# Kernel tuning notes

Hardware: AMD Instinct MI355X
Metric: run time of the kernel (lower is better)

Reference implementation:

```python
import jax, jax.numpy as jnp
import numpy as np

N_NODES = 20000
N_EDGES = 160000
N_GRAPHS = 64
DIMS = [9, 128, 256, 512, 1534]
NEG_SLOPE_ATT = 0.2   # GATConv attention LeakyReLU
NEG_SLOPE_ACT = 0.01  # nn.LeakyReLU between layers
EPS = 1e-5            # GraphNorm eps


def setup_inputs() -> dict:
    key = jax.random.key(0)
    inp = {}
    k, key = jax.random.split(key)
    inp['x'] = jax.random.normal(k, (N_NODES, DIMS[0]), jnp.float32)
    k, key = jax.random.split(key)
    inp['edge_index'] = jax.random.randint(k, (2, N_EDGES), 0, N_NODES)
    k, key = jax.random.split(key)
    inp['batch'] = jnp.sort(jax.random.randint(k, (N_NODES,), 0, N_GRAPHS))
    for l in range(4):
        din, dout = DIMS[l], DIMS[l + 1]
        k1, k2, k3, key = jax.random.split(key, 4)
        s = 1.0 / np.sqrt(din)
        inp[f'W{l}'] = (jax.random.normal(k1, (din, dout)) * s).astype(jnp.float32)
        inp[f'asrc{l}'] = (jax.random.normal(k2, (dout,)) * 0.1).astype(jnp.float32)
        inp[f'adst{l}'] = (jax.random.normal(k3, (dout,)) * 0.1).astype(jnp.float32)
        inp[f'b{l}'] = jnp.zeros((dout,), jnp.float32)
        inp[f'g{l}'] = jnp.ones((dout,), jnp.float32)   # GraphNorm weight
        inp[f'bt{l}'] = jnp.zeros((dout,), jnp.float32)  # GraphNorm bias
        inp[f'ms{l}'] = jnp.ones((dout,), jnp.float32)   # GraphNorm mean_scale
    return inp


def _gat_conv(h, src, dst, n, W, asrc, adst, b):
    # PyG GATConv, heads=1: linear (no bias), edge attention, segment softmax, scatter-add
    hp = h @ W                                                    # [N, dout]
    e = jax.nn.leaky_relu((hp @ asrc)[src] + (hp @ adst)[dst], NEG_SLOPE_ATT)  # [E]
    m = jax.ops.segment_max(e, dst, num_segments=n)
    m = jnp.where(jnp.isfinite(m), m, 0.0)
    ex = jnp.exp(e - m[dst])
    denom = jax.ops.segment_sum(ex, dst, num_segments=n)
    alpha = ex / (denom[dst] + 1e-16)                             # [E]
    out = jax.ops.segment_sum(alpha[:, None] * hp[src], dst, num_segments=n)
    return out + b


def _graph_norm(h, batch, counts, g, bt, ms):
    # PyG GraphNorm: per-graph mean/var with learnable mean_scale
    mean = jax.ops.segment_sum(h, batch, num_segments=N_GRAPHS) / counts
    out = h - ms * mean[batch]
    var = jax.ops.segment_sum(out * out, batch, num_segments=N_GRAPHS) / counts
    return out / jnp.sqrt(var[batch] + EPS) * g + bt


def _forward(x, edge_index, batch, params):
    n = x.shape[0]
    loops = jnp.arange(n)
    src = jnp.concatenate([edge_index[0], loops])   # GATConv add_self_loops=True
    dst = jnp.concatenate([edge_index[1], loops])
    counts = jax.ops.segment_sum(jnp.ones((n,), x.dtype), batch, num_segments=N_GRAPHS)[:, None]
    h = x
    for (W, asrc, adst, b, g, bt, ms) in params:
        h = _gat_conv(h, src, dst, n, W, asrc, adst, b)
        h = jax.nn.leaky_relu(h, NEG_SLOPE_ACT)
        h = _graph_norm(h, batch, counts, g, bt, ms)
        # Dropout(p=0.1) is identity in eval mode
    mean = (jax.ops.segment_sum(h, batch, num_segments=N_GRAPHS) / counts)[:, None, :]
    mx = jax.ops.segment_max(h, batch, num_segments=N_GRAPHS)[:, None, :]
    return jnp.concatenate([mean, mx], axis=1)      # [G, 2, 1534]


def reference(x, edge_index, batch,
              W0, asrc0, adst0, b0, g0, bt0, ms0,
              W1, asrc1, adst1, b1, g1, bt1, ms1,
              W2, asrc2, adst2, b2, g2, bt2, ms2,
              W3, asrc3, adst3, b3, g3, bt3, ms3):
    params = [
        (W0, asrc0, adst0, b0, g0, bt0, ms0),
        (W1, asrc1, adst1, b1, g1, bt1, ms1),
        (W2, asrc2, adst2, b2, g2, bt2, ms2),
        (W3, asrc3, adst3, b3, g3, bt3, ms3),
    ]
    return _forward(x, edge_index, batch, params)
```

## Files before the change

kernel.cpp:

```cpp
#include <hip/hip_runtime.h>
#include <math.h>

typedef unsigned int u32;
typedef unsigned short u16;
using half8 = __attribute__((ext_vector_type(8))) _Float16;
using f32x4 = __attribute__((ext_vector_type(4))) float;

#define NN 20000
#define MPAD 20096
#define NE 160000
#define ET 180000
#define NG 64
#define NBLK 79

constexpr float NEG_ATT = 0.2f;
constexpr float NEG_ACT = 0.01f;
constexpr float EPS_GN  = 1e-5f;

struct Ptr4 { const float *p0, *p1, *p2, *p3; };


__device__ __forceinline__ u16 f2h(float f) {
    _Float16 h = (_Float16)f;
    return __builtin_bit_cast(u16, h);
}
__device__ __forceinline__ float h2f(u16 b) {
    return (float)__builtin_bit_cast(_Float16, b);
}

__device__ __forceinline__ void gl_lds16(const void* g, void* l) {
    __builtin_amdgcn_global_load_lds((const __attribute__((address_space(1))) u32*)g,
                                     (__attribute__((address_space(3))) u32*)l, 16, 0, 0);
}

__device__ __forceinline__ float lrelu_att(float v) {
    return (v > 0.f) ? v : NEG_ATT * v;
}


__global__ void k_bounds(const int* __restrict__ batch, int* __restrict__ counts,
                         int* __restrict__ gstart) {
    __shared__ int ls[NG + 1];
    int g = threadIdx.x;
    int lo = 0, hi = NN;
    while (lo < hi) {
        int mid = (lo + hi) >> 1;
        if (batch[mid] < g) lo = mid + 1; else hi = mid;
    }
    ls[g] = lo;
    if (g == 0) ls[NG] = NN;
    __syncthreads();
    counts[g] = ls[g + 1] - ls[g];
    gstart[g] = ls[g];
    if (g == 0) gstart[NG] = NN;
}


__global__ void k_deg(const int* __restrict__ ei, int* deg) {
    int i = blockIdx.x * 256 + threadIdx.x;
    if (i >= ET) return;
    int dst = (i < NE) ? ei[NE + i] : (i - NE);
    atomicAdd(&deg[dst], 1);
}

__global__ void k_scan1(const int* __restrict__ deg, int* __restrict__ bsum) {
    int i = blockIdx.x * 256 + threadIdx.x;
    int v = (i < NN) ? deg[i] : 0;
    int lane = threadIdx.x & 63, w = threadIdx.x >> 6;
    #pragma unroll
    for (int off = 32; off; off >>= 1) v += __shfl_down(v, off, 64);
    __shared__ int ws[4];
    if (lane == 0) ws[w] = v;
    __syncthreads();
    if (threadIdx.x == 0) bsum[blockIdx.x] = ws[0] + ws[1] + ws[2] + ws[3];
}

__global__ void k_scan2(const int* __restrict__ bsum, int* __restrict__ boff,
                        int* __restrict__ total) {
    int tid = threadIdx.x;
    int v = (tid < NBLK) ? bsum[tid] : 0;
    int lane = tid & 63, w = tid >> 6;
    int val = v;
    #pragma unroll
    for (int off = 1; off < 64; off <<= 1) {
        int t = __shfl_up(val, off, 64);
        if (lane >= off) val += t;
    }
    __shared__ int ws[4];
    if (lane == 63) ws[w] = val;
    __syncthreads();
    int woff = 0;
    for (int k = 0; k < w; k++) woff += ws[k];
    int excl = woff + val - v;
    if (tid < NBLK) boff[tid] = excl;
    if (tid == NBLK - 1) *total = excl + v;
}

__global__ void k_scan3(const int* __restrict__ deg, const int* __restrict__ boff,
                        int* __restrict__ row_ptr, int* __restrict__ cursor) {
    int i = blockIdx.x * 256 + threadIdx.x;
    int v = (i < NN) ? deg[i] : 0;
    int lane = threadIdx.x & 63, w = threadIdx.x >> 6;
    int val = v;
    #pragma unroll
    for (int off = 1; off < 64; off <<= 1) {
        int t = __shfl_up(val, off, 64);
        if (lane >= off) val += t;
    }
    __shared__ int ws[4];
    if (lane == 63) ws[w] = val;
    __syncthreads();
    int woff = 0;
    for (int k = 0; k < w; k++) woff += ws[k];
    int excl = boff[blockIdx.x] + woff + val - v;
    if (i < NN) { row_ptr[i] = excl; cursor[i] = excl; }
}

__global__ void k_scatter(const int* __restrict__ ei, int* cursor, int* __restrict__ col) {
    int i = blockIdx.x * 256 + threadIdx.x;
    if (i >= ET) return;
    int s, d;
    if (i < NE) { s = ei[i]; d = ei[NE + i]; } else { s = i - NE; d = s; }
    int p = atomicAdd(&cursor[d], 1);
    col[p] = s;
}


__global__ void k_wvec_all(Ptr4 W, Ptr4 As, Ptr4 Ad,
                           float* __restrict__ wsrcA, float* __restrict__ wdstA) {
    const int dins[4]  = {9, 128, 256, 512};
    const int douts[4] = {128, 256, 512, 1534};
    int l = blockIdx.y, k = blockIdx.x;
    if (k >= dins[l]) return;
    const float* Wp = (l == 0) ? W.p0 : (l == 1) ? W.p1 : (l == 2) ? W.p2 : W.p3;
    const float* as = (l == 0) ? As.p0 : (l == 1) ? As.p1 : (l == 2) ? As.p2 : As.p3;
    const float* ad = (l == 0) ? Ad.p0 : (l == 1) ? Ad.p1 : (l == 2) ? Ad.p2 : Ad.p3;
    int NC = douts[l];
    const float* row = Wp + (size_t)k * NC;
    float ss = 0.f, sd = 0.f;
    for (int n = threadIdx.x; n < NC; n += 256) {
        float w = row[n];
        ss += w * as[n];
        sd += w * ad[n];
    }
    __shared__ float ls[8];
    int lane = threadIdx.x & 63, w4 = threadIdx.x >> 6;
    #pragma unroll
    for (int off = 32; off; off >>= 1) {
        ss += __shfl_down(ss, off, 64);
        sd += __shfl_down(sd, off, 64);
    }
    if (lane == 0) { ls[w4] = ss; ls[4 + w4] = sd; }
    __syncthreads();
    if (threadIdx.x == 0) {
        wsrcA[l * 512 + k] = ls[0] + ls[1] + ls[2] + ls[3];
        wdstA[l * 512 + k] = ls[4] + ls[5] + ls[6] + ls[7];
    }
}


__global__ void k_wbt_all(Ptr4 W, u16* __restrict__ WbTall) {
    const int Ks[3] = {128, 256, 512};
    const int NCs[3] = {256, 512, 1534};
    const int Nps[3] = {256, 512, 1536};
    const size_t offs[3] = {0, 256 * 128, 256 * 128 + 512 * 256};
    int l = blockIdx.z;
    int K = Ks[l], NC = NCs[l], Np = Nps[l];
    int n0 = blockIdx.x * 32, k0 = blockIdx.y * 32;
    if (n0 >= Np || k0 >= K) return;
    const float* Wp = (l == 0) ? W.p1 : (l == 1) ? W.p2 : W.p3;
    u16* WbT = WbTall + offs[l];
    __shared__ u16 tile[32][33];
    int tx = threadIdx.x & 31, ty = threadIdx.x >> 5;
    #pragma unroll
    for (int i = 0; i < 4; i++) {
        int k = k0 + ty + i * 8, n = n0 + tx;
        float v = (k < K && n < NC) ? Wp[(size_t)k * NC + n] : 0.f;
        tile[ty + i * 8][tx] = f2h(v);
    }
    __syncthreads();
    #pragma unroll
    for (int i = 0; i < 4; i++) {
        int n = n0 + ty + i * 8, k = k0 + tx;
        if (n < Np && k < K) WbT[(size_t)n * K + k] = tile[tx][ty + i * 8];
    }
}


__global__ void k_scores0(const float* __restrict__ x, const float* __restrict__ wsrc,
                          const float* __restrict__ wdst, float* __restrict__ s_src,
                          float* __restrict__ s_dst) {
    int v = blockIdx.x * 256 + threadIdx.x;
    if (v >= NN) return;
    const float* r = x + (size_t)v * 9;
    float ss = 0.f, sd = 0.f;
    #pragma unroll
    for (int k = 0; k < 9; k++) { ss += r[k] * wsrc[k]; sd += r[k] * wdst[k]; }
    s_src[v] = ss; s_dst[v] = sd;
}

template <int VW>
__global__ void k_scores_h(const u16* __restrict__ h, const float* __restrict__ wsrc,
                           const float* __restrict__ wdst, float* __restrict__ s_src,
                           float* __restrict__ s_dst, int din) {
    int v = blockIdx.x * 4 + (threadIdx.x >> 6);
    int lane = threadIdx.x & 63;
    if (v >= NN) return;
    const u16* row = h + (size_t)v * din;
    float ss = 0.f, sd = 0.f;
    for (int d = lane * VW; d < din; d += 64 * VW) {
        u32 ua[VW / 2];
        if constexpr (VW == 2) {
            ua[0] = *(const u32*)(row + d);
        } else if constexpr (VW == 4) {
            uint2 t = *(const uint2*)(row + d);
            ua[0] = t.x; ua[1] = t.y;
        } else {
            uint4 t = *(const uint4*)(row + d);
            ua[0] = t.x; ua[1] = t.y; ua[2] = t.z; ua[3] = t.w;
        }
        #pragma unroll
        for (int j = 0; j < VW / 2; j++) {
            float h0 = h2f((u16)(ua[j] & 0xffffu)), h1 = h2f((u16)(ua[j] >> 16));
            ss += h0 * wsrc[d + 2 * j] + h1 * wsrc[d + 2 * j + 1];
            sd += h0 * wdst[d + 2 * j] + h1 * wdst[d + 2 * j + 1];
        }
    }
    #pragma unroll
    for (int off = 32; off; off >>= 1) {
        ss += __shfl_down(ss, off, 64);
        sd += __shfl_down(sd, off, 64);
    }
    if (lane == 0) { s_src[v] = ss; s_dst[v] = sd; }
}


template <int TPN, int CPT>
__global__ __launch_bounds__(256) void k_agg_fused(const u16* __restrict__ h,
                                                   const int* __restrict__ row_ptr,
                                                   const int* __restrict__ col,
                                                   const float* __restrict__ s_src,
                                                   const float* __restrict__ s_dst,
                                                   u16* __restrict__ agg, int din) {
    constexpr int NPB = 256 / TPN;
    __shared__ float sm[NPB * 2];
    int grp = threadIdx.x / TPN;
    int lane = threadIdx.x % TPN;
    int v = blockIdx.x * NPB + grp;
    bool valid = v < NN;
    int st = 0, en = 0;
    float sd = 0.f;
    if (valid) { st = row_ptr[v]; en = row_ptr[v + 1]; sd = s_dst[v]; }

    float mx = -INFINITY;
    if (valid && lane < 64) {
        for (int p = st + lane; p < en; p += 64)
            mx = fmaxf(mx, lrelu_att(s_src[col[p]] + sd));
    }
    #pragma unroll
    for (int off = 32; off; off >>= 1) mx = fmaxf(mx, __shfl_xor(mx, off, 64));
    float sum = 0.f;
    if (valid && lane < 64) {
        for (int p = st + lane; p < en; p += 64)
            sum += __expf(lrelu_att(s_src[col[p]] + sd) - mx);
    }
    #pragma unroll
    for (int off = 32; off; off >>= 1) sum += __shfl_xor(sum, off, 64);
    if (lane == 0) { sm[grp * 2] = mx; sm[grp * 2 + 1] = 1.0f / (sum + 1e-16f); }
    __syncthreads();
    if (!valid) return;
    float m = sm[grp * 2], inv = sm[grp * 2 + 1];

    int d0 = lane * 2 * CPT;
    float acc[2 * CPT];
    #pragma unroll
    for (int i = 0; i < 2 * CPT; i++) acc[i] = 0.f;
    const u16* hb = h + d0;
    int p = st;
    for (; p + 2 <= en; p += 2) {
        int c0 = col[p], c1 = col[p + 1];
        float a0 = __expf(lrelu_att(s_src[c0] + sd) - m);
        float a1 = __expf(lrelu_att(s_src[c1] + sd) - m);
        u32 u0[CPT], u1[CPT];
        if constexpr (CPT == 1) {
            u0[0] = *(const u32*)(hb + (size_t)c0 * din);
            u1[0] = *(const u32*)(hb + (size_t)c1 * din);
        } else {
            uint2 t0 = *(const uint2*)(hb + (size_t)c0 * din);
            uint2 t1 = *(const uint2*)(hb + (size_t)c1 * din);
            u0[0] = t0.x; u0[1] = t0.y; u1[0] = t1.x; u1[1] = t1.y;
        }
        #pragma unroll
        for (int wv = 0; wv < CPT; wv++) {
            acc[2 * wv]     += a0 * h2f((u16)(u0[wv] & 0xffffu)) + a1 * h2f((u16)(u1[wv] & 0xffffu));
            acc[2 * wv + 1] += a0 * h2f((u16)(u0[wv] >> 16))     + a1 * h2f((u16)(u1[wv] >> 16));
        }
    }
    if (p < en) {
        int c0 = col[p];
        float a0 = __expf(lrelu_att(s_src[c0] + sd) - m);
        u32 u0[CPT];
        if constexpr (CPT == 1) {
            u0[0] = *(const u32*)(hb + (size_t)c0 * din);
        } else {
            uint2 t0 = *(const uint2*)(hb + (size_t)c0 * din);
            u0[0] = t0.x; u0[1] = t0.y;
        }
        #pragma unroll
        for (int wv = 0; wv < CPT; wv++) {
            acc[2 * wv]     += a0 * h2f((u16)(u0[wv] & 0xffffu));
            acc[2 * wv + 1] += a0 * h2f((u16)(u0[wv] >> 16));
        }
    }
    u32 o[CPT];
    #pragma unroll
    for (int wv = 0; wv < CPT; wv++)
        o[wv] = (u32)f2h(acc[2 * wv] * inv) | ((u32)f2h(acc[2 * wv + 1] * inv) << 16);
    if constexpr (CPT == 1) {
        *(u32*)(agg + (size_t)v * din + d0) = o[0];
    } else {
        uint2 ov; ov.x = o[0]; ov.y = o[1];
        *(uint2*)(agg + (size_t)v * din + d0) = ov;
    }
}

__global__ __launch_bounds__(256) void k_agg0_fused(const float* __restrict__ x,
                                                    const int* __restrict__ row_ptr,
                                                    const int* __restrict__ col,
                                                    const float* __restrict__ s_src,
                                                    const float* __restrict__ s_dst,
                                                    float* __restrict__ agg0) {
    __shared__ float sm[4 * 2];
    int grp = threadIdx.x >> 6;
    int lane = threadIdx.x & 63;
    int v = blockIdx.x * 4 + grp;
    bool valid = v < NN;
    int st = 0, en = 0;
    float sd = 0.f;
    if (valid) { st = row_ptr[v]; en = row_ptr[v + 1]; sd = s_dst[v]; }
    float mx = -INFINITY;
    if (valid) {
        for (int p = st + lane; p < en; p += 64)
            mx = fmaxf(mx, lrelu_att(s_src[col[p]] + sd));
    }
    #pragma unroll
    for (int off = 32; off; off >>= 1) mx = fmaxf(mx, __shfl_xor(mx, off, 64));
    float sum = 0.f;
    if (valid) {
        for (int p = st + lane; p < en; p += 64)
            sum += __expf(lrelu_att(s_src[col[p]] + sd) - mx);
    }
    #pragma unroll
    for (int off = 32; off; off >>= 1) sum += __shfl_xor(sum, off, 64);
    if (lane == 0) { sm[grp * 2] = mx; sm[grp * 2 + 1] = 1.0f / (sum + 1e-16f); }
    __syncthreads();
    if (!valid || lane >= 9) return;
    float m = sm[grp * 2], inv = sm[grp * 2 + 1];
    float acc = 0.f;
    for (int p = st; p < en; p++) {
        int c = col[p];
        float a = __expf(lrelu_att(s_src[c] + sd) - m);
        acc += a * x[(size_t)c * 9 + lane];
    }
    agg0[(size_t)v * 9 + lane] = acc * inv;
}


__global__ __launch_bounds__(256) void k_gemm0(const float* __restrict__ agg0,
                                               const float* __restrict__ W,
                                               const float* __restrict__ bias,
                                               u16* __restrict__ out) {
    __shared__ float Ws[9 * 128];
    for (int i = threadIdx.x; i < 9 * 128; i += 256) Ws[i] = W[i];
    __syncthreads();
    int node = blockIdx.x * 2 + (threadIdx.x >> 7);
    int n = threadIdx.x & 127;
    if (node >= NN) return;
    const float* xr = agg0 + (size_t)node * 9;
    float acc = bias[n];
    #pragma unroll
    for (int k = 0; k < 9; k++) acc += xr[k] * Ws[k * 128 + n];
    acc = (acc > 0.f) ? acc : NEG_ACT * acc;
    out[(size_t)node * 128 + n] = f2h(acc);
}


#define BM 128
#define BK 32

__global__ __launch_bounds__(256) void k_gemm_f16(const u16* __restrict__ A,
                                                  const u16* __restrict__ B,
                                                  const float* __restrict__ bias,
                                                  u16* __restrict__ C,
                                                  int K, int ldC, int NC, int ntx) {
    int nwg = gridDim.x;
    int b = blockIdx.x;
    int q = nwg >> 3, r = nwg & 7;
    int xcd = b & 7, idx = b >> 3;
    int wg = (xcd < r ? xcd * (q + 1) : r * (q + 1) + (xcd - r) * q) + idx;
    int row0 = (wg / ntx) * BM;
    int col0 = (wg % ntx) * BM;

    __shared__ u16 lds[2][2][BM * BK];
    int tid = threadIdx.x;
    int lane = tid & 63, w = tid >> 6;
    int wr = w >> 1, wc = w & 1;

    f32x4 acc[4][4];
    #pragma unroll
    for (int m = 0; m < 4; m++)
        #pragma unroll
        for (int n = 0; n < 4; n++)
            #pragma unroll
            for (int rr2 = 0; rr2 < 4; rr2++) acc[m][n][rr2] = 0.f;

    int nt = K / BK;

    auto stage = [&](int buf, int t) {
        int k0 = t * BK;
        #pragma unroll
        for (int c = 0; c < 2; c++) {
            int idx2 = tid + c * 256;
            int rr2 = idx2 >> 2, kc = idx2 & 3;
            int kcs = kc ^ (rr2 & 3);
            gl_lds16(A + (size_t)(row0 + rr2) * K + k0 + kcs * 8, &lds[buf][0][idx2 * 8]);
            gl_lds16(B + (size_t)(col0 + rr2) * K + k0 + kcs * 8, &lds[buf][1][idx2 * 8]);
        }
    };

    auto compute = [&](int buf) {
        const u16* As = &lds[buf][0][0];
        const u16* Bs = &lds[buf][1][0];
        int kg = lane >> 4, rl = lane & 15;
        half8 af[4], bfr[4];
        #pragma unroll
        for (int m = 0; m < 4; m++) {
            int rr2 = wr * 64 + m * 16 + rl;
            af[m] = *(const half8*)(As + rr2 * BK + (kg ^ (rr2 & 3)) * 8);
        }
        #pragma unroll
        for (int n = 0; n < 4; n++) {
            int rr2 = wc * 64 + n * 16 + rl;
            bfr[n] = *(const half8*)(Bs + rr2 * BK + (kg ^ (rr2 & 3)) * 8);
        }
        #pragma unroll
        for (int m = 0; m < 4; m++)
            #pragma unroll
            for (int n = 0; n < 4; n++)
                acc[m][n] = __builtin_amdgcn_mfma_f32_16x16x32_f16(af[m], bfr[n], acc[m][n], 0, 0, 0);
    };

    stage(0, 0);
    __syncthreads();
    for (int t = 0; t < nt; t++) {
        if (t + 1 < nt) stage((t + 1) & 1, t + 1);
        compute(t & 1);
        __syncthreads();
    }

    u16* ep = ((u16*)lds) + w * (32 * 72);
    int kg = lane >> 4, rl = lane & 15;
    int rrow = lane >> 3;
    int c8 = (lane & 7) * 8;
    #pragma unroll
    for (int half = 0; half < 2; half++) {
        #pragma unroll
        for (int m2 = 0; m2 < 2; m2++) {
            int m = half * 2 + m2;
            #pragma unroll
            for (int n = 0; n < 4; n++) {
                int colg = col0 + wc * 64 + n * 16 + rl;
                float bb = (colg < NC) ? bias[colg] : 0.f;
                #pragma unroll
                for (int rr2 = 0; rr2 < 4; rr2++) {
                    float o = acc[m][n][rr2] + bb;
                    o = (o > 0.f) ? o : NEG_ACT * o;
                    ep[(m2 * 16 + kg * 4 + rr2) * 72 + n * 16 + rl] = f2h(o);
                }
            }
        }
        #pragma unroll
        for (int it = 0; it < 4; it++) {
            int rloc = it * 8 + rrow;
            half8 vv = *(const half8*)(ep + rloc * 72 + c8);
            int rowg = row0 + wr * 64 + half * 32 + rloc;
            *(half8*)(C + (size_t)rowg * ldC + col0 + wc * 64 + c8) = vv;
        }
    }
}


__global__ __launch_bounds__(1024, 4) void k_gemm256(const u16* __restrict__ A,
                                                     const u16* __restrict__ B,
                                                     const float* __restrict__ bias,
                                                     u16* __restrict__ C,
                                                     int K, int ldC, int NC, int ntx, int M) {
    __shared__ u16 sMem[49152];

    int nwg = gridDim.x, b = blockIdx.x;
    int q = nwg >> 3, r = nwg & 7;
    int xcd = b & 7, bidx = b >> 3;
    int wg = (xcd < r ? xcd * (q + 1) : r * (q + 1) + (xcd - r) * q) + bidx;
    int row0 = (wg / ntx) * 256;
    int col0 = (wg % ntx) * 256;

    int tid = threadIdx.x;
    int w = tid >> 6, lane = tid & 63;
    int wm = w >> 2, wn = w & 3;
    int rl = lane & 15, kg = lane >> 4;
    int ksl = (kg ^ ((rl >> 1) & 3)) * 8;

    f32x4 acc[4][4];
    #pragma unroll
    for (int m = 0; m < 4; m++)
        #pragma unroll
        for (int n = 0; n < 4; n++)
            #pragma unroll
            for (int i = 0; i < 4; i++) acc[m][n][i] = 0.f;

    {
        int rr = tid >> 2, s = tid & 3;
        int ss = s ^ ((rr >> 1) & 3);
        int ra = row0 + rr; ra = (ra < M) ? ra : (M - 1);
        const u16* aSrc0 = A + (size_t)ra * K + ss * 8;
        const u16* bSrc0 = B + (size_t)(col0 + rr) * K + ss * 8;
        u16* dstA = sMem + tid * 8;
        u16* dstB = sMem + 8192 + tid * 8;

        auto stage = [&](int t, int bf2) {
            gl_lds16(aSrc0 + t * 32, dstA + bf2 * 16384);
            gl_lds16(bSrc0 + t * 32, dstB + bf2 * 16384);
        };

        half8 af[4], bf[4];
        auto ldAB = [&](int bf2) {
            const u16* Ab = sMem + bf2 * 16384;
            const u16* Bb = Ab + 8192;
            #pragma unroll
            for (int i = 0; i < 4; i++)
                af[i] = *(const half8*)(Ab + (wm * 64 + i * 16 + rl) * 32 + ksl);
            #pragma unroll
            for (int i = 0; i < 4; i++)
                bf[i] = *(const half8*)(Bb + (wn * 64 + i * 16 + rl) * 32 + ksl);
        };

        int nt = K >> 5;

        stage(0, 0); stage(1, 1);
        __builtin_amdgcn_sched_barrier(0);
        asm volatile("s_waitcnt vmcnt(2)" ::: "memory");
        __builtin_amdgcn_s_barrier();
        __builtin_amdgcn_sched_barrier(0);

        int rb = 0;
        for (int t = 0; t < nt; t++) {
            int sb = rb + 2; if (sb >= 3) sb -= 3;
            if (t + 2 < nt) stage(t + 2, sb);
            ldAB(rb);
            __builtin_amdgcn_s_setprio(1);
            #pragma unroll
            for (int i = 0; i < 4; i++)
                #pragma unroll
                for (int n = 0; n < 4; n++)
                    acc[i][n] = __builtin_amdgcn_mfma_f32_16x16x32_f16(af[i], bf[n], acc[i][n], 0, 0, 0);
            __builtin_amdgcn_s_setprio(0);
            __builtin_amdgcn_sched_barrier(0);
            if (t + 2 < nt)      asm volatile("s_waitcnt vmcnt(2)" ::: "memory");
            else if (t + 1 < nt) asm volatile("s_waitcnt vmcnt(0)" ::: "memory");
            __builtin_amdgcn_s_barrier();
            __builtin_amdgcn_sched_barrier(0);
            rb = (rb == 2) ? 0 : rb + 1;
        }
    }

    u16* ep = sMem + w * (32 * 72);
    float bv[4];
    #pragma unroll
    for (int n = 0; n < 4; n++) {
        int colg = col0 + wn * 64 + n * 16 + rl;
        bv[n] = (colg < NC) ? bias[colg] : 0.f;
    }
    int rrow = lane >> 3, c8 = (lane & 7) * 8;
    #pragma unroll
    for (int mh = 0; mh < 2; mh++) {
        #pragma unroll
        for (int msub = 0; msub < 2; msub++) {
            int m = mh * 2 + msub;
            #pragma unroll
            for (int n = 0; n < 4; n++) {
                #pragma unroll
                for (int rg = 0; rg < 4; rg++) {
                    float o = acc[m][n][rg] + bv[n];
                    o = (o > 0.f) ? o : NEG_ACT * o;
                    ep[(msub * 16 + kg * 4 + rg) * 72 + n * 16 + rl] = f2h(o);
                }
            }
        }
        #pragma unroll
        for (int it = 0; it < 4; it++) {
            int rloc = it * 8 + rrow;
            half8 vv = *(const half8*)(ep + rloc * 72 + c8);
            int rowg = row0 + wm * 64 + mh * 32 + rloc;
            if (rowg < M)
                *(half8*)(C + (size_t)rowg * ldC + col0 + wn * 64 + c8) = vv;
        }
    }
}


__global__ __launch_bounds__(256) void k_gn_fused(const u16* __restrict__ h,
                           const int* __restrict__ gstart,
                           const float* __restrict__ ms, const float* __restrict__ gam,
                           const float* __restrict__ bet, u16* __restrict__ out, int ld) {
    int g = blockIdx.x;
    int c0 = blockIdx.y * 128;
    int ct = threadIdx.x & 15, rg = threadIdx.x >> 4;
    int d0 = c0 + ct * 8;
    int st = gstart[g], en = gstart[g + 1];
    float inv = 1.0f / (float)(en - st);
    float s[8], qq[8];
    #pragma unroll
    for (int i = 0; i < 8; i++) { s[i] = 0.f; qq[i] = 0.f; }
    for (int r = st + rg; r < en; r += 16) {
        uint4 u = *(const uint4*)(h + (size_t)r * ld + d0);
        u32 ua[4] = {u.x, u.y, u.z, u.w};
        #pragma unroll
        for (int j = 0; j < 4; j++) {
            float v0 = h2f((u16)(ua[j] & 0xffffu)), v1 = h2f((u16)(ua[j] >> 16));
            s[2 * j] += v0; s[2 * j + 1] += v1;
            qq[2 * j] += v0 * v0; qq[2 * j + 1] += v1 * v1;
        }
    }
    __shared__ float Ls[16][128], Lq[16][128];
    #pragma unroll
    for (int i = 0; i < 8; i++) { Ls[rg][ct * 8 + i] = s[i]; Lq[rg][ct * 8 + i] = qq[i]; }
    __syncthreads();
    int tid = threadIdx.x;
    if (tid < 128) {
        float ss = 0.f, sq = 0.f;
        #pragma unroll
        for (int r2 = 1; r2 < 16; r2++) { ss += Ls[r2][tid]; sq += Lq[r2][tid]; }
        Ls[0][tid] += ss; Lq[0][tid] += sq;
    }
    __syncthreads();
    float sub[8], sc[8], bv[8];
    #pragma unroll
    for (int i = 0; i < 8; i++) {
        int cl = ct * 8 + i, d = d0 + i;
        float msv = ms[d];
        float mean = Ls[0][cl] * inv;
        float q2   = Lq[0][cl] * inv;
        float var  = fmaxf(q2 - (2.f * msv - msv * msv) * mean * mean, 0.f);
        sub[i] = msv * mean;
        sc[i]  = gam[d] * rsqrtf(var + EPS_GN);
        bv[i]  = bet[d];
    }
    for (int r = st + rg; r < en; r += 16) {
        uint4 u = *(const uint4*)(h + (size_t)r * ld + d0);
        u32 ua[4] = {u.x, u.y, u.z, u.w};
        uint4 wv4;
        u32 wo[4];
        #pragma unroll
        for (int j = 0; j < 4; j++) {
            float o0 = (h2f((u16)(ua[j] & 0xffffu)) - sub[2 * j]) * sc[2 * j] + bv[2 * j];
            float o1 = (h2f((u16)(ua[j] >> 16)) - sub[2 * j + 1]) * sc[2 * j + 1] + bv[2 * j + 1];
            wo[j] = (u32)f2h(o0) | ((u32)f2h(o1) << 16);
        }
        wv4.x = wo[0]; wv4.y = wo[1]; wv4.z = wo[2]; wv4.w = wo[3];
        *(uint4*)(out + (size_t)r * ld + d0) = wv4;
    }
}

__global__ __launch_bounds__(256) void k_gn_poolf(const u16* __restrict__ h,
                           const int* __restrict__ gstart,
                           const float* __restrict__ ms, const float* __restrict__ gam,
                           const float* __restrict__ bet, float* __restrict__ out,
                           int dout, int ld) {
    int g = blockIdx.x;
    int c0 = blockIdx.y * 128;
    int ct = threadIdx.x & 15, rg = threadIdx.x >> 4;
    int d0 = c0 + ct * 8;
    int st = gstart[g], en = gstart[g + 1];
    float inv = 1.0f / (float)(en - st);
    float s[8], qq[8];
    #pragma unroll
    for (int i = 0; i < 8; i++) { s[i] = 0.f; qq[i] = 0.f; }
    for (int r = st + rg; r < en; r += 16) {
        uint4 u = *(const uint4*)(h + (size_t)r * ld + d0);
        u32 ua[4] = {u.x, u.y, u.z, u.w};
        #pragma unroll
        for (int j = 0; j < 4; j++) {
            float v0 = h2f((u16)(ua[j] & 0xffffu)), v1 = h2f((u16)(ua[j] >> 16));
            s[2 * j] += v0; s[2 * j + 1] += v1;
            qq[2 * j] += v0 * v0; qq[2 * j + 1] += v1 * v1;
        }
    }
    __shared__ float Ls[16][128], Lq[16][128];
    #pragma unroll
    for (int i = 0; i < 8; i++) { Ls[rg][ct * 8 + i] = s[i]; Lq[rg][ct * 8 + i] = qq[i]; }
    __syncthreads();
    int tid = threadIdx.x;
    if (tid < 128) {
        float ss = 0.f, sq = 0.f;
        #pragma unroll
        for (int r2 = 1; r2 < 16; r2++) { ss += Ls[r2][tid]; sq += Lq[r2][tid]; }
        Ls[0][tid] += ss; Lq[0][tid] += sq;
    }
    __syncthreads();
    float sub[8], sc[8], bv[8];
    #pragma unroll
    for (int i = 0; i < 8; i++) {
        int cl = ct * 8 + i, d = d0 + i;
        int dc = (d < dout) ? d : (dout - 1);
        float msv = ms[dc];
        float mean = Ls[0][cl] * inv;
        float q2   = Lq[0][cl] * inv;
        float var  = fmaxf(q2 - (2.f * msv - msv * msv) * mean * mean, 0.f);
        sub[i] = msv * mean;
        sc[i]  = gam[dc] * rsqrtf(var + EPS_GN);
        bv[i]  = bet[dc];
    }
    float ps[8], pm[8];
    #pragma unroll
    for (int i = 0; i < 8; i++) { ps[i] = 0.f; pm[i] = -INFINITY; }
    for (int r = st + rg; r < en; r += 16) {
        uint4 u = *(const uint4*)(h + (size_t)r * ld + d0);
        u32 ua[4] = {u.x, u.y, u.z, u.w};
        #pragma unroll
        for (int j = 0; j < 4; j++) {
            float o0 = (h2f((u16)(ua[j] & 0xffffu)) - sub[2 * j]) * sc[2 * j] + bv[2 * j];
            float o1 = (h2f((u16)(ua[j] >> 16)) - sub[2 * j + 1]) * sc[2 * j + 1] + bv[2 * j + 1];
            ps[2 * j] += o0; ps[2 * j + 1] += o1;
            pm[2 * j] = fmaxf(pm[2 * j], o0); pm[2 * j + 1] = fmaxf(pm[2 * j + 1], o1);
        }
    }
    __syncthreads();
    #pragma unroll
    for (int i = 0; i < 8; i++) { Ls[rg][ct * 8 + i] = ps[i]; Lq[rg][ct * 8 + i] = pm[i]; }
    __syncthreads();
    if (tid < 128) {
        float ss = 0.f, mm = -INFINITY;
        #pragma unroll
        for (int r2 = 0; r2 < 16; r2++) { ss += Ls[r2][tid]; mm = fmaxf(mm, Lq[r2][tid]); }
        int d = c0 + tid;
        if (d < dout) {
            out[(size_t)g * 2 * dout + d] = ss * inv;
            out[(size_t)g * 2 * dout + dout + d] = mm;
        }
    }
}


extern "C" void kernel_launch(void* const* d_in, const int* in_sizes, int n_in,
                              void* d_out, int out_size, void* d_ws, size_t ws_size,
                              hipStream_t stream) {
    const float* x = (const float*)d_in[0];
    const int* ei = (const int*)d_in[1];
    const int* batch = (const int*)d_in[2];
    const float *Wl[4], *Asr[4], *Ads[4], *Bi[4], *Ga[4], *Be[4], *Ms[4];
    for (int l = 0; l < 4; l++) {
        int b = 3 + 7 * l;
        Wl[l]  = (const float*)d_in[b];
        Asr[l] = (const float*)d_in[b + 1];
        Ads[l] = (const float*)d_in[b + 2];
        Bi[l]  = (const float*)d_in[b + 3];
        Ga[l]  = (const float*)d_in[b + 4];
        Be[l]  = (const float*)d_in[b + 5];
        Ms[l]  = (const float*)d_in[b + 6];
    }

    char* ws = (char*)d_ws;
    size_t off = 0;
    auto alloc = [&](size_t bytes) -> char* {
        char* p = ws + off;
        off += (bytes + 255) & ~(size_t)255;
        return p;
    };
    u16*   actA   = (u16*)alloc((size_t)MPAD * 512 * 2);
    u16*   actB   = (u16*)alloc((size_t)MPAD * 1536 * 2);
    u16*   agg    = (u16*)alloc((size_t)MPAD * 512 * 2);
    float* agg0   = (float*)alloc((size_t)NN * 9 * 4);
    u16*   WbTall = (u16*)alloc((size_t)(256 * 128 + 512 * 256 + 1536 * 512) * 2);
    float* wsrcA  = (float*)alloc((size_t)4 * 512 * 4);
    float* wdstA  = (float*)alloc((size_t)4 * 512 * 4);
    float* s_src  = (float*)alloc((size_t)NN * 4);
    float* s_dst  = (float*)alloc((size_t)NN * 4);
    int* row_ptr  = (int*)alloc((size_t)(NN + 1) * 4);
    int* cursor   = (int*)alloc((size_t)NN * 4);
    int* colA     = (int*)alloc((size_t)ET * 4);
    int* counts   = (int*)alloc((size_t)NG * 4);
    int* gstart   = (int*)alloc((size_t)(NG + 1) * 4);
    int* bsum     = (int*)alloc((size_t)NBLK * 4);
    int* boff     = (int*)alloc((size_t)NBLK * 4);

    char* zbase = ws + off;
    int* deg      = (int*)alloc((size_t)NN * 4);
    size_t zbytes = (size_t)((ws + off) - zbase);
    hipMemsetAsync(zbase, 0, zbytes, stream);

    k_bounds<<<1, 64, 0, stream>>>(batch, counts, gstart);
    k_deg<<<(ET + 255) / 256, 256, 0, stream>>>(ei, deg);
    k_scan1<<<NBLK, 256, 0, stream>>>(deg, bsum);
    k_scan2<<<1, 256, 0, stream>>>(bsum, boff, row_ptr + NN);
    k_scan3<<<NBLK, 256, 0, stream>>>(deg, boff, row_ptr, cursor);
    k_scatter<<<(ET + 255) / 256, 256, 0, stream>>>(ei, cursor, colA);

    Ptr4 Wp{Wl[0], Wl[1], Wl[2], Wl[3]};
    Ptr4 Ap{Asr[0], Asr[1], Asr[2], Asr[3]};
    Ptr4 Dp{Ads[0], Ads[1], Ads[2], Ads[3]};
    k_wvec_all<<<dim3(512, 4), 256, 0, stream>>>(Wp, Ap, Dp, wsrcA, wdstA);
    k_wbt_all<<<dim3(48, 16, 3), 256, 0, stream>>>(Wp, WbTall);

    const int dims[5] = {9, 128, 256, 512, 1534};
    const size_t wbtOffs[3] = {0, 256 * 128, 256 * 128 + 512 * 256};
    const int RT256 = (MPAD + 255) / 256;

    for (int l = 0; l < 4; l++) {
        int din = dims[l], dout = dims[l + 1];
        int ldo = (dout == 1534) ? 1536 : dout;
        const float* wsrc = wsrcA + l * 512;
        const float* wdst = wdstA + l * 512;

        if (l == 0) {
            k_scores0<<<(NN + 255) / 256, 256, 0, stream>>>(x, wsrc, wdst, s_src, s_dst);
            k_agg0_fused<<<(NN + 3) / 4, 256, 0, stream>>>(x, row_ptr, colA, s_src, s_dst, agg0);
            k_gemm0<<<(NN + 1) / 2, 256, 0, stream>>>(agg0, Wl[0], Bi[0], actB);
        } else if (l == 1) {
            k_scores_h<2><<<(NN + 3) / 4, 256, 0, stream>>>(actA, wsrc, wdst, s_src, s_dst, din);
            k_agg_fused<64, 1><<<(NN + 3) / 4, 256, 0, stream>>>(actA, row_ptr, colA, s_src, s_dst, agg, din);
            int ntx = ldo / 128;
            int nwg = ntx * (MPAD / 128);
            k_gemm_f16<<<nwg, 256, 0, stream>>>(agg, WbTall + wbtOffs[0], Bi[1], actB,
                                                din, ldo, dout, ntx);
        } else {
            if (din == 256) {
                k_scores_h<4><<<(NN + 3) / 4, 256, 0, stream>>>(actA, wsrc, wdst, s_src, s_dst, din);
                k_agg_fused<64, 2><<<(NN + 3) / 4, 256, 0, stream>>>(actA, row_ptr, colA, s_src, s_dst, agg, din);
            } else {
                k_scores_h<8><<<(NN + 3) / 4, 256, 0, stream>>>(actA, wsrc, wdst, s_src, s_dst, din);
                k_agg_fused<128, 2><<<(NN + 1) / 2, 256, 0, stream>>>(actA, row_ptr, colA, s_src, s_dst, agg, din);
            }
            int ntx = ldo / 256;
            int nwg = ntx * RT256;
            k_gemm256<<<nwg, 1024, 0, stream>>>(agg, WbTall + wbtOffs[l - 1], Bi[l], actB,
                                                din, ldo, dout, ntx, MPAD);
        }

        if (l < 3)
            k_gn_fused<<<dim3(NG, ldo / 128), 256, 0, stream>>>(actB, gstart,
                                                                Ms[l], Ga[l], Be[l], actA, ldo);
        else
            k_gn_poolf<<<dim3(NG, 12), 256, 0, stream>>>(actB, gstart,
                                                         Ms[3], Ga[3], Be[3], (float*)d_out,
                                                         1534, 1536);
    }
}
```

Before: 332.9 us.

## Split GAT aggregation into alpha precompute and column-chunked gather kernels

The fused softmax+aggregation kernel is replaced by two kernels. The first computes per-edge normalized attention weights into a global buffer, and the second gathers neighbor features in 64-column chunks with 16 threads per node and 16 nodes per block. This removes the repeated exp/score recomputation per feature lane and the block-level sync, and gives many more small blocks with better occupancy. In exchange it adds an extra launch, an alpha buffer write and read, and repeated col/alpha reads for each column chunk.

```diff
diff --git a/kernel.cpp b/kernel.cpp
--- a/kernel.cpp
+++ b/kernel.cpp
@@ -235,93 +235,74 @@
 }
 
 
-template <int TPN, int CPT>
-__global__ __launch_bounds__(256) void k_agg_fused(const u16* __restrict__ h,
-                                                   const int* __restrict__ row_ptr,
-                                                   const int* __restrict__ col,
-                                                   const float* __restrict__ s_src,
-                                                   const float* __restrict__ s_dst,
-                                                   u16* __restrict__ agg, int din) {
-    constexpr int NPB = 256 / TPN;
-    __shared__ float sm[NPB * 2];
-    int grp = threadIdx.x / TPN;
-    int lane = threadIdx.x % TPN;
-    int v = blockIdx.x * NPB + grp;
-    bool valid = v < NN;
-    int st = 0, en = 0;
-    float sd = 0.f;
-    if (valid) { st = row_ptr[v]; en = row_ptr[v + 1]; sd = s_dst[v]; }
-
+__global__ __launch_bounds__(256) void k_alpha(const int* __restrict__ row_ptr,
+                                               const int* __restrict__ col,
+                                               const float* __restrict__ s_src,
+                                               const float* __restrict__ s_dst,
+                                               float* __restrict__ alpha) {
+    int grp = threadIdx.x >> 6;
+    int lane = threadIdx.x & 63;
+    int v = blockIdx.x * 4 + grp;
+    if (v >= NN) return;
+    int st = row_ptr[v], en = row_ptr[v + 1];
+    float sd = s_dst[v];
     float mx = -INFINITY;
-    if (valid && lane < 64) {
-        for (int p = st + lane; p < en; p += 64)
-            mx = fmaxf(mx, lrelu_att(s_src[col[p]] + sd));
-    }
+    for (int p = st + lane; p < en; p += 64)
+        mx = fmaxf(mx, lrelu_att(s_src[col[p]] + sd));
     #pragma unroll
     for (int off = 32; off; off >>= 1) mx = fmaxf(mx, __shfl_xor(mx, off, 64));
     float sum = 0.f;
-    if (valid && lane < 64) {
-        for (int p = st + lane; p < en; p += 64)
-            sum += __expf(lrelu_att(s_src[col[p]] + sd) - mx);
-    }
+    for (int p = st + lane; p < en; p += 64)
+        sum += __expf(lrelu_att(s_src[col[p]] + sd) - mx);
     #pragma unroll
     for (int off = 32; off; off >>= 1) sum += __shfl_xor(sum, off, 64);
-    if (lane == 0) { sm[grp * 2] = mx; sm[grp * 2 + 1] = 1.0f / (sum + 1e-16f); }
-    __syncthreads();
-    if (!valid) return;
-    float m = sm[grp * 2], inv = sm[grp * 2 + 1];
-
-    int d0 = lane * 2 * CPT;
-    float acc[2 * CPT];
-    #pragma unroll
-    for (int i = 0; i < 2 * CPT; i++) acc[i] = 0.f;
+    float inv = 1.0f / (sum + 1e-16f);
+    for (int p = st + lane; p < en; p += 64)
+        alpha[p] = __expf(lrelu_att(s_src[col[p]] + sd) - mx) * inv;
+}
+
+
+__global__ __launch_bounds__(256) void k_agg_gather(const u16* __restrict__ h,
+                                                    const int* __restrict__ row_ptr,
+                                                    const int* __restrict__ col,
+                                                    const float* __restrict__ alpha,
+                                                    u16* __restrict__ agg,
+                                                    int din, int nbn) {
+    int blk = blockIdx.x;
+    int chunk = blk / nbn;
+    int nb = blk % nbn;
+    int tg = threadIdx.x >> 4;
+    int lane = threadIdx.x & 15;
+    int v = nb * 16 + tg;
+    if (v >= NN) return;
+    int st = row_ptr[v], en = row_ptr[v + 1];
+    int d0 = chunk * 64 + lane * 4;
     const u16* hb = h + d0;
+    float a0_, a1_, acc0 = 0.f, acc1 = 0.f, acc2 = 0.f, acc3 = 0.f;
     int p = st;
     for (; p + 2 <= en; p += 2) {
         int c0 = col[p], c1 = col[p + 1];
-        float a0 = __expf(lrelu_att(s_src[c0] + sd) - m);
-        float a1 = __expf(lrelu_att(s_src[c1] + sd) - m);
-        u32 u0[CPT], u1[CPT];
-        if constexpr (CPT == 1) {
-            u0[0] = *(const u32*)(hb + (size_t)c0 * din);
-            u1[0] = *(const u32*)(hb + (size_t)c1 * din);
-        } else {
-            uint2 t0 = *(const uint2*)(hb + (size_t)c0 * din);
-            uint2 t1 = *(const uint2*)(hb + (size_t)c1 * din);
-            u0[0] = t0.x; u0[1] = t0.y; u1[0] = t1.x; u1[1] = t1.y;
-        }
-        #pragma unroll
-        for (int wv = 0; wv < CPT; wv++) {
-            acc[2 * wv]     += a0 * h2f((u16)(u0[wv] & 0xffffu)) + a1 * h2f((u16)(u1[wv] & 0xffffu));
-            acc[2 * wv + 1] += a0 * h2f((u16)(u0[wv] >> 16))     + a1 * h2f((u16)(u1[wv] >> 16));
-        }
+        a0_ = alpha[p]; a1_ = alpha[p + 1];
+        uint2 t0 = *(const uint2*)(hb + (size_t)c0 * din);
+        uint2 t1 = *(const uint2*)(hb + (size_t)c1 * din);
+        acc0 += a0_ * h2f((u16)(t0.x & 0xffffu)) + a1_ * h2f((u16)(t1.x & 0xffffu));
+        acc1 += a0_ * h2f((u16)(t0.x >> 16))     + a1_ * h2f((u16)(t1.x >> 16));
+        acc2 += a0_ * h2f((u16)(t0.y & 0xffffu)) + a1_ * h2f((u16)(t1.y & 0xffffu));
+        acc3 += a0_ * h2f((u16)(t0.y >> 16))     + a1_ * h2f((u16)(t1.y >> 16));
     }
     if (p < en) {
         int c0 = col[p];
-        float a0 = __expf(lrelu_att(s_src[c0] + sd) - m);
-        u32 u0[CPT];
-        if constexpr (CPT == 1) {
-            u0[0] = *(const u32*)(hb + (size_t)c0 * din);
-        } else {
-            uint2 t0 = *(const uint2*)(hb + (size_t)c0 * din);
-            u0[0] = t0.x; u0[1] = t0.y;
-        }
-        #pragma unroll
-        for (int wv = 0; wv < CPT; wv++) {
-            acc[2 * wv]     += a0 * h2f((u16)(u0[wv] & 0xffffu));
-            acc[2 * wv + 1] += a0 * h2f((u16)(u0[wv] >> 16));
-        }
-    }
-    u32 o[CPT];
-    #pragma unroll
-    for (int wv = 0; wv < CPT; wv++)
-        o[wv] = (u32)f2h(acc[2 * wv] * inv) | ((u32)f2h(acc[2 * wv + 1] * inv) << 16);
-    if constexpr (CPT == 1) {
-        *(u32*)(agg + (size_t)v * din + d0) = o[0];
-    } else {
-        uint2 ov; ov.x = o[0]; ov.y = o[1];
-        *(uint2*)(agg + (size_t)v * din + d0) = ov;
-    }
+        a0_ = alpha[p];
+        uint2 t0 = *(const uint2*)(hb + (size_t)c0 * din);
+        acc0 += a0_ * h2f((u16)(t0.x & 0xffffu));
+        acc1 += a0_ * h2f((u16)(t0.x >> 16));
+        acc2 += a0_ * h2f((u16)(t0.y & 0xffffu));
+        acc3 += a0_ * h2f((u16)(t0.y >> 16));
+    }
+    uint2 ov;
+    ov.x = (u32)f2h(acc0) | ((u32)f2h(acc1) << 16);
+    ov.y = (u32)f2h(acc2) | ((u32)f2h(acc3) << 16);
+    *(uint2*)(agg + (size_t)v * din + d0) = ov;
 }
 
 __global__ __launch_bounds__(256) void k_agg0_fused(const float* __restrict__ x,
@@ -785,6 +766,7 @@
     float* wdstA  = (float*)alloc((size_t)4 * 512 * 4);
     float* s_src  = (float*)alloc((size_t)NN * 4);
     float* s_dst  = (float*)alloc((size_t)NN * 4);
+    float* alpha  = (float*)alloc((size_t)ET * 4);
     int* row_ptr  = (int*)alloc((size_t)(NN + 1) * 4);
     int* cursor   = (int*)alloc((size_t)NN * 4);
     int* colA     = (int*)alloc((size_t)ET * 4);
@@ -814,6 +796,7 @@
     const int dims[5] = {9, 128, 256, 512, 1534};
     const size_t wbtOffs[3] = {0, 256 * 128, 256 * 128 + 512 * 256};
     const int RT256 = (MPAD + 255) / 256;
+    const int NBN = (NN + 15) / 16;
 
     for (int l = 0; l < 4; l++) {
         int din = dims[l], dout = dims[l + 1];
@@ -825,25 +808,28 @@
             k_scores0<<<(NN + 255) / 256, 256, 0, stream>>>(x, wsrc, wdst, s_src, s_dst);
             k_agg0_fused<<<(NN + 3) / 4, 256, 0, stream>>>(x, row_ptr, colA, s_src, s_dst, agg0);
             k_gemm0<<<(NN + 1) / 2, 256, 0, stream>>>(agg0, Wl[0], Bi[0], actB);
-        } else if (l == 1) {
-            k_scores_h<2><<<(NN + 3) / 4, 256, 0, stream>>>(actA, wsrc, wdst, s_src, s_dst, din);
-            k_agg_fused<64, 1><<<(NN + 3) / 4, 256, 0, stream>>>(actA, row_ptr, colA, s_src, s_dst, agg, din);
-            int ntx = ldo / 128;
-            int nwg = ntx * (MPAD / 128);
-            k_gemm_f16<<<nwg, 256, 0, stream>>>(agg, WbTall + wbtOffs[0], Bi[1], actB,
-                                                din, ldo, dout, ntx);
         } else {
-            if (din == 256) {
+            if (din == 128)
+                k_scores_h<2><<<(NN + 3) / 4, 256, 0, stream>>>(actA, wsrc, wdst, s_src, s_dst, din);
+            else if (din == 256)
                 k_scores_h<4><<<(NN + 3) / 4, 256, 0, stream>>>(actA, wsrc, wdst, s_src, s_dst, din);
-                k_agg_fused<64, 2><<<(NN + 3) / 4, 256, 0, stream>>>(actA, row_ptr, colA, s_src, s_dst, agg, din);
+            else
+                k_scores_h<8><<<(NN + 3) / 4, 256, 0, stream>>>(actA, wsrc, wdst, s_src, s_dst, din);
+            k_alpha<<<(NN + 3) / 4, 256, 0, stream>>>(row_ptr, colA, s_src, s_dst, alpha);
+            int nchunks = din / 64;
+            k_agg_gather<<<nchunks * NBN, 256, 0, stream>>>(actA, row_ptr, colA, alpha,
+                                                            agg, din, NBN);
+            if (l == 1) {
+                int ntx = ldo / 128;
+                int nwg = ntx * (MPAD / 128);
+                k_gemm_f16<<<nwg, 256, 0, stream>>>(agg, WbTall + wbtOffs[0], Bi[1], actB,
+                                                    din, ldo, dout, ntx);
             } else {
-                k_scores_h<8><<<(NN + 3) / 4, 256, 0, stream>>>(actA, wsrc, wdst, s_src, s_dst, din);
-                k_agg_fused<128, 2><<<(NN + 1) / 2, 256, 0, stream>>>(actA, row_ptr, colA, s_src, s_dst, agg, din);
+                int ntx = ldo / 256;
+                int nwg = ntx * RT256;
+                k_gemm256<<<nwg, 1024, 0, stream>>>(agg, WbTall + wbtOffs[l - 1], Bi[l], actB,
+                                                    din, ldo, dout, ntx, MPAD);
             }
-            int ntx = ldo / 256;
-            int nwg = ntx * RT256;
-            k_gemm256<<<nwg, 1024, 0, stream>>>(agg, WbTall + wbtOffs[l - 1], Bi[l], actB,
-                                                din, ldo, dout, ntx, MPAD);
         }
 
         if (l < 3)
```

New measurement: 343.8 us. 3.3% more time.
